# Performance work log

Measured on AMD Instinct MI355X. Metric: run time of the kernel, lower is better.

Reference implementation:

```python
import jax, jax.numpy as jnp
import numpy as np

B, N, NS, D, H, DH, K, R = 16, 4096, 24, 512, 8, 64, 512, 8
ITERS = 3
EPS = 1e-8
LORA_SCALE = 8.0


def setup_inputs() -> dict:
    key = jax.random.key(0)
    ks = jax.random.split(key, 16)
    rn = lambda k, shape, s=0.02: jax.random.normal(k, shape, jnp.float32) * s
    return {
        "inputs": jax.random.normal(ks[0], (B, N, D), jnp.float32),
        "conditioning": jax.random.normal(ks[1], (B, NS, D), jnp.float32),
        "Wq": rn(ks[2], (D, D)),
        "Wk": rn(ks[3], (D, D)),
        "Wv": rn(ks[4], (D, D)),
        "gru_w_ih": rn(ks[5], (3 * D, D)),
        "gru_w_hh": rn(ks[6], (3 * D, D)),
        "gru_b_ih": jnp.zeros((3 * D,), jnp.float32),
        "gru_b_hh": jnp.zeros((3 * D,), jnp.float32),
        "ln_in_g": jnp.ones((D,), jnp.float32),
        "ln_in_b": jnp.zeros((D,), jnp.float32),
        "ln_s_g": jnp.ones((D,), jnp.float32),
        "ln_s_b": jnp.zeros((D,), jnp.float32),
        "ln_f_g": jnp.ones((D,), jnp.float32),
        "ln_f_b": jnp.zeros((D,), jnp.float32),
        "W1": rn(ks[7], (D, 4 * D)),
        "b1": jnp.zeros((4 * D,), jnp.float32),
        "W2": rn(ks[8], (4 * D, D)),
        "b2": jnp.zeros((D,), jnp.float32),
        "A1": rn(ks[9], (K, D, R)),
        "B1": rn(ks[10], (K, R, 4 * D)),
        "A2": rn(ks[11], (K, 4 * D, R)),
        "B2": rn(ks[12], (K, R, D)),
        "codebook": jax.random.normal(ks[13], (K, D), jnp.float32),
    }


def _ln(x, g, b):
    m = x.mean(-1, keepdims=True)
    v = ((x - m) ** 2).mean(-1, keepdims=True)
    return (x - m) * jax.lax.rsqrt(v + 1e-5) * g + b


def _lora(x, idx, A, Bm):
    # AdaLoRA: per-slot adapter selected by VQ index.  idx: [b, ns] int
    t = jnp.einsum('bnd,bndr->bnr', x, A[idx])          # [b,ns,r]
    return jnp.einsum('bnr,bnro->bno', t, Bm[idx]) * (LORA_SCALE / R)


def _vq(slots, codebook):
    d2 = (jnp.sum(slots ** 2, -1, keepdims=True)
          - 2.0 * jnp.einsum('bnd,kd->bnk', slots, codebook)
          + jnp.sum(codebook ** 2, -1))                 # [b,ns,K]
    idx = jnp.argmin(d2, axis=-1)                       # [b,ns]
    q = codebook[idx]
    commit = jnp.mean((slots - jax.lax.stop_gradient(q)) ** 2)
    return idx, commit


def _gru(x, h, w_ih, w_hh, b_ih, b_hh):
    gi = x @ w_ih.T + b_ih
    gh = h @ w_hh.T + b_hh
    ir, iz, inn = jnp.split(gi, 3, axis=-1)
    hr, hz, hn = jnp.split(gh, 3, axis=-1)
    r = jax.nn.sigmoid(ir + hr)
    z = jax.nn.sigmoid(iz + hz)
    n = jnp.tanh(inn + r * hn)
    return (1.0 - z) * n + z * h


def reference(inputs, conditioning, Wq, Wk, Wv, gru_w_ih, gru_w_hh, gru_b_ih,
              gru_b_hh, ln_in_g, ln_in_b, ln_s_g, ln_s_b, ln_f_g, ln_f_b,
              W1, b1, W2, b2, A1, B1, A2, B2, codebook):
    scale = DH ** -0.5
    x = _ln(inputs, ln_in_g, ln_in_b)
    # mod_position='f': k/v/q LoRAs are ZeroModule, so k/v are identical
    # across iterations -> compute once (same math as the torch loop).
    k = (x @ Wk).reshape(B, N, H, DH)
    v = (x @ Wv).reshape(B, N, H, DH)
    slots = conditioning
    indices = None
    commit = jnp.float32(0.0)
    for i in range(ITERS):
        idx = None
        if i > 0:
            indices, commit = _vq(slots, codebook)
            idx = indices
        slots_prev = slots
        s = _ln(slots, ln_s_g, ln_s_b)
        q = (s @ Wq).reshape(B, NS, H, DH)
        dots = jnp.einsum('bihd,bjhd->bihj', q, k) * scale      # [b,ns,h,n]
        a = jax.nn.softmax(dots.reshape(B, NS * H, N), axis=1).reshape(B, NS, H, N)
        attn_bw = a
        a = a + EPS
        a = a / a.sum(-1, keepdims=True)
        upd = jnp.einsum('bjhd,bihj->bihd', v, a).reshape(B * NS, D)
        slots = _gru(upd, slots_prev.reshape(B * NS, D),
                     gru_w_ih, gru_w_hh, gru_b_ih, gru_b_hh).reshape(B, NS, D)
        slots_prev_ff = slots
        s2 = _ln(slots, ln_f_g, ln_f_b)
        h1 = s2 @ W1 + b1
        if idx is not None:
            h1 = h1 + _lora(s2, idx, A1, B1)
        h1 = jax.nn.relu(h1)
        out = h1 @ W2 + b2
        if idx is not None:
            out = out + _lora(h1, idx, A2, B2)
        slots = out + slots_prev_ff
        attn = attn_bw.mean(axis=2)                              # [b,ns,n]
    return slots, attn, indices, commit, indices
```

## Files before the change

### kernel.cpp

```cpp
#include <hip/hip_runtime.h>
#include <hip/hip_bf16.h>
#include <math.h>


#define B_ 16
#define N_ 4096
#define NS_ 24
#define D_ 512
#define H_ 8
#define DH_ 64
#define KC_ 512
#define R_ 8
#define TT_ (NS_*H_)
#define EPS_ 1e-8f
#define BNSD_ (B_*NS_*D_)
#define M_ 384

typedef unsigned short u16x8 __attribute__((ext_vector_type(8)));
typedef short s16x8 __attribute__((ext_vector_type(8)));
typedef float f32x4 __attribute__((ext_vector_type(4)));

__device__ inline unsigned short f2bf(float f) {
  unsigned int u = __float_as_uint(f);
  u += 0x7FFFu + ((u >> 16) & 1u);
  return (unsigned short)(u >> 16);
}
__device__ inline float bf2f(unsigned short h) {
  return __uint_as_float(((unsigned int)h) << 16);
}

__global__ __launch_bounds__(128) void ln_hl_kernel(const float* __restrict__ X,
    const float* __restrict__ g, const float* __restrict__ bb,
    unsigned short* __restrict__ Y)
{
  int row = blockIdx.x;
  const float* xr = X + (size_t)row * D_;
  int t = threadIdx.x;
  float lv[4];
#pragma unroll
  for (int i = 0; i < 4; ++i) lv[i] = xr[t + 128 * i];
  float s = lv[0] + lv[1] + lv[2] + lv[3];
#pragma unroll
  for (int o = 1; o < 64; o <<= 1) s += __shfl_xor(s, o);
  __shared__ float sh[2], sh2[2];
  if ((t & 63) == 0) sh[t >> 6] = s;
  __syncthreads();
  float mean = (sh[0] + sh[1]) * (1.f / D_);
  float q = 0.f;
#pragma unroll
  for (int i = 0; i < 4; ++i) { float d = lv[i] - mean; q += d * d; }
#pragma unroll
  for (int o = 1; o < 64; o <<= 1) q += __shfl_xor(q, o);
  if ((t & 63) == 0) sh2[t >> 6] = q;
  __syncthreads();
  float var = (sh2[0] + sh2[1]) * (1.f / D_);
  float rstd = 1.0f / sqrtf(var + 1e-5f);
#pragma unroll
  for (int i = 0; i < 4; ++i) {
    int d = t + 128 * i;
    float y = (lv[i] - mean) * rstd * g[d] + bb[d];
    unsigned short h = f2bf(y);
    unsigned short l = f2bf(y - bf2f(h));
    Y[(size_t)row * 1024 + d] = h;
    Y[(size_t)row * 1024 + 512 + d] = l;
  }
}

__global__ __launch_bounds__(128) void ln_dual_kernel(const float* __restrict__ X,
    const float* __restrict__ g, const float* __restrict__ bb,
    float* __restrict__ Yf, unsigned short* __restrict__ Yhl)
{
  int row = blockIdx.x;
  const float* xr = X + (size_t)row * D_;
  int t = threadIdx.x;
  float lv[4];
#pragma unroll
  for (int i = 0; i < 4; ++i) lv[i] = xr[t + 128 * i];
  float s = lv[0] + lv[1] + lv[2] + lv[3];
#pragma unroll
  for (int o = 1; o < 64; o <<= 1) s += __shfl_xor(s, o);
  __shared__ float sh[2], sh2[2];
  if ((t & 63) == 0) sh[t >> 6] = s;
  __syncthreads();
  float mean = (sh[0] + sh[1]) * (1.f / D_);
  float q = 0.f;
#pragma unroll
  for (int i = 0; i < 4; ++i) { float d = lv[i] - mean; q += d * d; }
#pragma unroll
  for (int o = 1; o < 64; o <<= 1) q += __shfl_xor(q, o);
  if ((t & 63) == 0) sh2[t >> 6] = q;
  __syncthreads();
  float var = (sh2[0] + sh2[1]) * (1.f / D_);
  float rstd = 1.0f / sqrtf(var + 1e-5f);
#pragma unroll
  for (int i = 0; i < 4; ++i) {
    int d = t + 128 * i;
    float y = (lv[i] - mean) * rstd * g[d] + bb[d];
    Yf[(size_t)row * D_ + d] = y;
    unsigned short h = f2bf(y);
    unsigned short l = f2bf(y - bf2f(h));
    Yhl[(size_t)row * 1024 + d] = h;
    Yhl[(size_t)row * 1024 + 512 + d] = l;
  }
}

__global__ __launch_bounds__(256) void wtrans_g(const float* __restrict__ W,
    unsigned short* __restrict__ WT, int K, int N)
{
  __shared__ float t[64][65];
  int n0 = blockIdx.x * 64, k0 = blockIdx.y * 64;
  for (int e = threadIdx.x; e < 4096; e += 256) {
    int kk = e >> 6, nn = e & 63;
    t[kk][nn] = W[(size_t)(k0 + kk) * N + n0 + nn];
  }
  __syncthreads();
  for (int e = threadIdx.x; e < 4096; e += 256) {
    int nn = e >> 6, kk = e & 63;
    float v = t[kk][nn];
    unsigned short h = f2bf(v);
    unsigned short l = f2bf(v - bf2f(h));
    size_t base = (size_t)(n0 + nn) * 3 * K + (k0 + kk);
    WT[base] = h; WT[base + K] = h; WT[base + 2 * K] = l;
  }
}

__global__ __launch_bounds__(256) void wsplit_nm(const float* __restrict__ W,
    unsigned short* __restrict__ WT, int K, int total)
{
  int e = blockIdx.x * 256 + threadIdx.x;
  if (e >= total) return;
  int n = e / K, k = e % K;
  float v = W[e];
  unsigned short h = f2bf(v);
  unsigned short l = f2bf(v - bf2f(h));
  size_t base = (size_t)n * 3 * K + k;
  WT[base] = h; WT[base + K] = h; WT[base + 2 * K] = l;
}

__global__ __launch_bounds__(256) void f32tohl_kernel(const float* __restrict__ X,
    float* __restrict__ Cout, unsigned short* __restrict__ HL, int total)
{
  int e = blockIdx.x * 256 + threadIdx.x;
  if (e >= total) return;
  float v = X[e];
  if (Cout) Cout[e] = v;
  int m = e >> 9, d = e & 511;
  unsigned short h = f2bf(v);
  unsigned short l = f2bf(v - bf2f(h));
  HL[(size_t)m * 1024 + d] = h;
  HL[(size_t)m * 1024 + 512 + d] = l;
}

__global__ __launch_bounds__(256) void reluhl_kernel(const float* __restrict__ X,
    unsigned short* __restrict__ HL)
{
  int e = blockIdx.x * 256 + threadIdx.x;
  float v = fmaxf(X[e], 0.f);
  int m = e >> 11, d = e & 2047;
  unsigned short h = f2bf(v);
  unsigned short l = f2bf(v - bf2f(h));
  HL[(size_t)m * 4096 + d] = h;
  HL[(size_t)m * 4096 + 2048 + d] = l;
}

__global__ __launch_bounds__(256) void gemm_kv(
    const unsigned short* __restrict__ A, const unsigned short* __restrict__ BT,
    float* __restrict__ C)
{
  __shared__ unsigned short As[128 * 64];
  __shared__ unsigned short Bs[128 * 64];
  const int tid = threadIdx.x;
  const int lane = tid & 63, wid = tid >> 6;
  const int wm = wid >> 1, wn = wid & 1;
  const int g = lane >> 4, r16 = lane & 15;
  const int m0 = blockIdx.y * 128, n0 = blockIdx.x * 128;

  f32x4 acc[4][4] = {};
  u16x8 ra[4], rb[4];
  int srow[4], sj[4];
#pragma unroll
  for (int i = 0; i < 4; ++i) {
    int s = tid + (i << 8);
    srow[i] = s >> 3;
    sj[i] = (s & 7) ^ (srow[i] & 7);
  }
#pragma unroll
  for (int i = 0; i < 4; ++i) {
    ra[i] = *(const u16x8*)(A + (size_t)(m0 + srow[i]) * 1024 + (sj[i] << 3));
    rb[i] = *(const u16x8*)(BT + (size_t)(n0 + srow[i]) * 1536 + (sj[i] << 3));
  }
  u16x8* Asw = (u16x8*)As;
  u16x8* Bsw = (u16x8*)Bs;
  const s16x8* Asv = (const s16x8*)As;
  const s16x8* Bsv = (const s16x8*)Bs;

  for (int kk = 0; kk < 24; ++kk) {
    __syncthreads();
#pragma unroll
    for (int i = 0; i < 4; ++i) {
      Asw[tid + (i << 8)] = ra[i];
      Bsw[tid + (i << 8)] = rb[i];
    }
    __syncthreads();
    if (kk + 1 < 24) {
      int k2 = kk + 1;
      int acol = ((k2 < 16) ? k2 : (k2 - 16)) * 64;
      int bcol = k2 * 64;
#pragma unroll
      for (int i = 0; i < 4; ++i) {
        ra[i] = *(const u16x8*)(A + (size_t)(m0 + srow[i]) * 1024 + acol + (sj[i] << 3));
        rb[i] = *(const u16x8*)(BT + (size_t)(n0 + srow[i]) * 1536 + bcol + (sj[i] << 3));
      }
    }
#pragma unroll
    for (int kh = 0; kh < 2; ++kh) {
      s16x8 af[4], bfr[4];
      int j = kh * 4 + g;
#pragma unroll
      for (int mi = 0; mi < 4; ++mi) {
        int m = wm * 64 + mi * 16 + r16;
        af[mi] = Asv[m * 8 + (j ^ (m & 7))];
      }
#pragma unroll
      for (int ni = 0; ni < 4; ++ni) {
        int n = wn * 64 + ni * 16 + r16;
        bfr[ni] = Bsv[n * 8 + (j ^ (n & 7))];
      }
#pragma unroll
      for (int mi = 0; mi < 4; ++mi)
#pragma unroll
        for (int ni = 0; ni < 4; ++ni)
          acc[mi][ni] = __builtin_amdgcn_mfma_f32_16x16x32_bf16(
              af[mi], bfr[ni], acc[mi][ni], 0, 0, 0);
    }
  }
#pragma unroll
  for (int mi = 0; mi < 4; ++mi) {
    int mrow = m0 + wm * 64 + mi * 16 + g * 4;
#pragma unroll
    for (int ni = 0; ni < 4; ++ni) {
      int ncol = n0 + wn * 64 + ni * 16 + r16;
#pragma unroll
      for (int j = 0; j < 4; ++j)
        C[(size_t)(mrow + j) * 512 + ncol] = acc[mi][ni][j];
    }
  }
}

__global__ __launch_bounds__(256) void gemm_sp(
    const unsigned short* __restrict__ A, const unsigned short* __restrict__ WT,
    float* __restrict__ part, int N, int K, int S)
{
  __shared__ unsigned short As[128 * 64];
  __shared__ unsigned short Bs[64 * 64];
  const int tid = threadIdx.x;
  const int lane = tid & 63, wid = tid >> 6;
  const int wm = wid >> 1, wn = wid & 1;
  const int g = lane >> 4, r16 = lane & 15;
  const int n0 = blockIdx.x * 64, m0 = blockIdx.y * 128, z = blockIdx.z;
  const int twoK = 2 * K;
  const size_t ldb = (size_t)3 * K;

  f32x4 acc[4][2] = {};
  u16x8 ra[4], rb[2];
  int arow[4], aj[4], brow[2], bj[2];
#pragma unroll
  for (int i = 0; i < 4; ++i) {
    int s = tid + (i << 8);
    arow[i] = s >> 3; aj[i] = (s & 7) ^ (arow[i] & 7);
  }
#pragma unroll
  for (int i = 0; i < 2; ++i) {
    int s = tid + (i << 8);
    brow[i] = s >> 3; bj[i] = (s & 7) ^ (brow[i] & 7);
  }
  const int s0 = z * S;
  {
    int c = s0 * 64;
    int ac = (c < twoK) ? c : c - twoK;
#pragma unroll
    for (int i = 0; i < 4; ++i)
      ra[i] = *(const u16x8*)(A + (size_t)(m0 + arow[i]) * twoK + ac + (aj[i] << 3));
#pragma unroll
    for (int i = 0; i < 2; ++i)
      rb[i] = *(const u16x8*)(WT + (size_t)(n0 + brow[i]) * ldb + c + (bj[i] << 3));
  }
  u16x8* Asw = (u16x8*)As;
  u16x8* Bsw = (u16x8*)Bs;
  const s16x8* Asv = (const s16x8*)As;
  const s16x8* Bsv = (const s16x8*)Bs;

  for (int st = 0; st < S; ++st) {
    __syncthreads();
#pragma unroll
    for (int i = 0; i < 4; ++i) Asw[tid + (i << 8)] = ra[i];
#pragma unroll
    for (int i = 0; i < 2; ++i) Bsw[tid + (i << 8)] = rb[i];
    __syncthreads();
    if (st + 1 < S) {
      int c = (s0 + st + 1) * 64;
      int ac = (c < twoK) ? c : c - twoK;
#pragma unroll
      for (int i = 0; i < 4; ++i)
        ra[i] = *(const u16x8*)(A + (size_t)(m0 + arow[i]) * twoK + ac + (aj[i] << 3));
#pragma unroll
      for (int i = 0; i < 2; ++i)
        rb[i] = *(const u16x8*)(WT + (size_t)(n0 + brow[i]) * ldb + c + (bj[i] << 3));
    }
#pragma unroll
    for (int kh = 0; kh < 2; ++kh) {
      int j = kh * 4 + g;
      s16x8 af[4], bf2v[2];
#pragma unroll
      for (int mi = 0; mi < 4; ++mi) {
        int m = wm * 64 + mi * 16 + r16;
        af[mi] = Asv[m * 8 + (j ^ (m & 7))];
      }
#pragma unroll
      for (int ni = 0; ni < 2; ++ni) {
        int n = wn * 32 + ni * 16 + r16;
        bf2v[ni] = Bsv[n * 8 + (j ^ (n & 7))];
      }
#pragma unroll
      for (int mi = 0; mi < 4; ++mi)
#pragma unroll
        for (int ni = 0; ni < 2; ++ni)
          acc[mi][ni] = __builtin_amdgcn_mfma_f32_16x16x32_bf16(
              af[mi], bf2v[ni], acc[mi][ni], 0, 0, 0);
    }
  }
  size_t zb = (size_t)z * M_ * N;
#pragma unroll
  for (int mi = 0; mi < 4; ++mi) {
    int mr = m0 + wm * 64 + mi * 16 + g * 4;
#pragma unroll
    for (int ni = 0; ni < 2; ++ni) {
      int nc = n0 + wn * 32 + ni * 16 + r16;
#pragma unroll
      for (int j2 = 0; j2 < 4; ++j2)
        part[zb + (size_t)(mr + j2) * N + nc] = acc[mi][ni][j2];
    }
  }
}

template<bool BIAS, bool RES, bool WHL>
__global__ __launch_bounds__(256) void redep(const float* __restrict__ part,
    const float* __restrict__ bias, const float* __restrict__ res,
    float* __restrict__ C, unsigned short* __restrict__ HL, int N, int Z)
{
  int e = blockIdx.x * 256 + threadIdx.x;
  size_t MN = (size_t)M_ * N;
  float v = 0.f;
  for (int z = 0; z < Z; ++z) v += part[(size_t)z * MN + e];
  int m = e / N, n = e - m * N;
  if (BIAS) v += bias[n];
  if (RES) v += res[e];
  C[e] = v;
  if (WHL) {
    unsigned short h = f2bf(v), l = f2bf(v - bf2f(h));
    HL[(size_t)m * 2 * N + n] = h;
    HL[(size_t)m * 2 * N + N + n] = l;
  }
}

__global__ __launch_bounds__(256) void vsum_kernel(const float* __restrict__ v,
                                                   float* __restrict__ vsum)
{
  int b = blockIdx.x >> 3, h = blockIdx.x & 7;
  int dh = threadIdx.x & 63, w = threadIdx.x >> 6;
  float acc = 0.f;
  for (int j = w * (N_ / 4); j < (w + 1) * (N_ / 4); ++j)
    acc += v[((size_t)b * N_ + j) * D_ + h * 64 + dh];
  __shared__ float sh[4][64];
  sh[w][dh] = acc;
  __syncthreads();
  if (w == 0)
    vsum[(size_t)blockIdx.x * 64 + dh] = sh[0][dh] + sh[1][dh] + sh[2][dh] + sh[3][dh];
}

__global__ __launch_bounds__(256) void vq_kernel(const float* __restrict__ slots,
    const float* __restrict__ cb, int* __restrict__ idx, float* __restrict__ commit)
{
  __shared__ float ss[D_];
  int slot = blockIdx.x;
  const float* sr = slots + (size_t)slot * D_;
  for (int d = threadIdx.x; d < D_; d += 256) ss[d] = sr[d];
  __syncthreads();
  float best = 1e30f; int bi = 0;
  for (int c = threadIdx.x; c < KC_; c += 256) {
    const float* cr = cb + (size_t)c * D_;
    float d2 = 0.f;
    for (int d = 0; d < D_; ++d) { float df = ss[d] - cr[d]; d2 += df * df; }
    if (d2 < best) { best = d2; bi = c; }
  }
  __shared__ float rb[256]; __shared__ int ri[256];
  rb[threadIdx.x] = best; ri[threadIdx.x] = bi;
  __syncthreads();
  for (int s = 128; s > 0; s >>= 1) {
    if (threadIdx.x < s) {
      float ob = rb[threadIdx.x + s]; int oi = ri[threadIdx.x + s];
      if (ob < rb[threadIdx.x] || (ob == rb[threadIdx.x] && oi < ri[threadIdx.x])) {
        rb[threadIdx.x] = ob; ri[threadIdx.x] = oi;
      }
    }
    __syncthreads();
  }
  if (threadIdx.x == 0) {
    idx[slot] = ri[0];
    atomicAdd(commit, rb[0] * (1.f / (B_ * NS_ * D_)));
  }
}

__global__ __launch_bounds__(256) void dots_kernel(const float* __restrict__ q,
    const float* __restrict__ k, float* __restrict__ dots)
{
  int b = blockIdx.y >> 3, h = blockIdx.y & 7;
  int j0 = blockIdx.x * 64;
  __shared__ float qs[NS_][DH_];
  __shared__ float ks[64][DH_ + 1];
  for (int e = threadIdx.x; e < NS_ * DH_; e += 256) {
    int i = e >> 6, dh = e & 63;
    qs[i][dh] = q[(size_t)(b * NS_ + i) * D_ + h * 64 + dh];
  }
  for (int e = threadIdx.x; e < 64 * 64; e += 256) {
    int jj = e >> 6, dh = e & 63;
    ks[jj][dh] = k[((size_t)b * N_ + j0 + jj) * D_ + h * 64 + dh];
  }
  __syncthreads();
  int jj = threadIdx.x & 63;
  int ib = threadIdx.x >> 6;
  float acc[6] = {0.f, 0.f, 0.f, 0.f, 0.f, 0.f};
  for (int dh = 0; dh < 64; ++dh) {
    float kv = ks[jj][dh];
#pragma unroll
    for (int ii = 0; ii < 6; ++ii) acc[ii] += qs[ii * 4 + ib][dh] * kv;
  }
#pragma unroll
  for (int ii = 0; ii < 6; ++ii) {
    int i = ii * 4 + ib;
    dots[((size_t)(b * NS_ + i) * H_ + h) * N_ + j0 + jj] = acc[ii] * 0.125f;
  }
}

__global__ __launch_bounds__(256) void softmax_kernel(float* __restrict__ dots,
    float* __restrict__ asum, float* __restrict__ attn)
{
  int b = blockIdx.y;
  int j = blockIdx.x * 256 + threadIdx.x;
  size_t base = (size_t)b * TT_ * N_ + j;
  float m = -1e30f;
  for (int t = 0; t < TT_; ++t) m = fmaxf(m, dots[base + (size_t)t * N_]);
  float S = 0.f;
  for (int t = 0; t < TT_; ++t) S += __expf(dots[base + (size_t)t * N_] - m);
  float rinv = 1.f / S;
  float am[NS_];
#pragma unroll
  for (int i = 0; i < NS_; ++i) am[i] = 0.f;
  for (int t = 0; t < TT_; ++t) {
    float w = __expf(dots[base + (size_t)t * N_] - m) * rinv;
    dots[base + (size_t)t * N_] = w;
    am[t >> 3] += w;
    float wsum = w;
#pragma unroll
    for (int o = 1; o < 64; o <<= 1) wsum += __shfl_xor(wsum, o);
    if ((threadIdx.x & 63) == 0) atomicAdd(&asum[b * TT_ + t], wsum);
  }
  if (attn) {
    for (int i = 0; i < NS_; ++i)
      attn[((size_t)b * NS_ + i) * N_ + j] = am[i] * (1.f / H_);
  }
}

__global__ __launch_bounds__(256) void upd_part_kernel(const float* __restrict__ a,
    const float* __restrict__ v, float* __restrict__ part)
{
  int bh = blockIdx.x;
  int c = blockIdx.y;
  int b = bh >> 3, h = bh & 7;
  __shared__ float vs[64][DH_ + 1];
  __shared__ float as[NS_][64];
  int dh = threadIdx.x & 63;
  int ib = threadIdx.x >> 6;
  float acc[6] = {0.f, 0.f, 0.f, 0.f, 0.f, 0.f};
  for (int j0 = c * 1024; j0 < (c + 1) * 1024; j0 += 64) {
    __syncthreads();
    for (int e = threadIdx.x; e < 64 * 64; e += 256) {
      int jj = e >> 6, d2 = e & 63;
      vs[jj][d2] = v[((size_t)b * N_ + j0 + jj) * D_ + h * 64 + d2];
    }
    for (int e = threadIdx.x; e < NS_ * 64; e += 256) {
      int i = e >> 6, jj = e & 63;
      as[i][jj] = a[((size_t)(b * NS_ + i) * H_ + h) * N_ + j0 + jj];
    }
    __syncthreads();
    for (int jj = 0; jj < 64; ++jj) {
      float vv = vs[jj][dh];
#pragma unroll
      for (int ii = 0; ii < 6; ++ii) acc[ii] += as[ii * 4 + ib][jj] * vv;
    }
  }
#pragma unroll
  for (int ii = 0; ii < 6; ++ii) {
    int i = ii * 4 + ib;
    part[((size_t)c * B_ * NS_ + b * NS_ + i) * D_ + h * 64 + dh] = acc[ii];
  }
}

__global__ __launch_bounds__(256) void upd_fin_kernel(const float* __restrict__ part,
    const float* __restrict__ vsum, const float* __restrict__ asum,
    unsigned short* __restrict__ updhl)
{
  int e = blockIdx.x * 256 + threadIdx.x;
  int d = e & 511, bi = e >> 9;
  int b = bi / NS_, h = d >> 6, dh = d & 63;
  float s = part[e] + part[BNSD_ + e] + part[2 * BNSD_ + e] + part[3 * BNSD_ + e];
  float dnm = asum[bi * H_ + h] + (float)N_ * EPS_;
  float val = (s + EPS_ * vsum[(b * H_ + h) * 64 + dh]) / dnm;
  unsigned short hh = f2bf(val), ll = f2bf(val - bf2f(hh));
  updhl[(size_t)bi * 1024 + d] = hh;
  updhl[(size_t)bi * 1024 + 512 + d] = ll;
}

__global__ __launch_bounds__(256) void gru_kernel(const float* __restrict__ gi,
    const float* __restrict__ gh, const float* __restrict__ h, float* __restrict__ out)
{
  int e = blockIdx.x * 256 + threadIdx.x;
  int row = e >> 9, d = e & 511;
  const float* gir = gi + (size_t)row * 1536;
  const float* ghr = gh + (size_t)row * 1536;
  float ir = gir[d], iz = gir[512 + d], inn = gir[1024 + d];
  float hr = ghr[d], hz = ghr[512 + d], hn = ghr[1024 + d];
  float r = 1.f / (1.f + __expf(-(ir + hr)));
  float z = 1.f / (1.f + __expf(-(iz + hz)));
  float n = tanhf(inn + r * hn);
  out[e] = (1.f - z) * n + z * h[e];
}

template<bool RELU_X>
__global__ __launch_bounds__(256) void lora_kernel(const float* __restrict__ x,
    const float* __restrict__ Am, const float* __restrict__ Bm,
    const int* __restrict__ idx, float* __restrict__ out, int Din, int Dout)
{
  int slot = blockIdx.x;
  int code = idx[slot];
  const float* xr = x + (size_t)slot * Din;
  const float* Ar = Am + (size_t)code * Din * R_;
  const float* Br = Bm + (size_t)code * R_ * Dout;
  float part[R_];
#pragma unroll
  for (int r = 0; r < R_; ++r) part[r] = 0.f;
  for (int d = threadIdx.x; d < Din; d += 256) {
    float xv = xr[d];
    if (RELU_X) xv = fmaxf(xv, 0.f);
#pragma unroll
    for (int r = 0; r < R_; ++r) part[r] += xv * Ar[(size_t)d * R_ + r];
  }
#pragma unroll
  for (int r = 0; r < R_; ++r)
#pragma unroll
    for (int o = 1; o < 64; o <<= 1) part[r] += __shfl_xor(part[r], o);
  __shared__ float tsh[4][R_];
  __shared__ float tfin[R_];
  int wave = threadIdx.x >> 6, lane = threadIdx.x & 63;
  if (lane == 0)
    for (int r = 0; r < R_; ++r) tsh[wave][r] = part[r];
  __syncthreads();
  if (threadIdx.x < R_)
    tfin[threadIdx.x] = (tsh[0][threadIdx.x] + tsh[1][threadIdx.x] +
                         tsh[2][threadIdx.x] + tsh[3][threadIdx.x]);
  __syncthreads();
  for (int c = threadIdx.x; c < Dout; c += 256) {
    float acc = 0.f;
#pragma unroll
    for (int r = 0; r < R_; ++r) acc += tfin[r] * Br[(size_t)r * Dout + c];
    out[(size_t)slot * Dout + c] += acc;
  }
}

__global__ __launch_bounds__(256) void finalize_kernel(const float* __restrict__ slots,
    const int* __restrict__ idx, const float* __restrict__ commit, float* __restrict__ out)
{
  int t = blockIdx.x * 256 + threadIdx.x;
  if (t < B_ * NS_ * D_) out[t] = slots[t];
  if (t < B_ * NS_) {
    float iv = (float)idx[t];
    out[1769472 + t] = iv;
    out[1769857 + t] = iv;
  }
  if (t == 0) out[1769856] = commit[0];
}

extern "C" void kernel_launch(void* const* d_in, const int* in_sizes, int n_in,
                              void* d_out, int out_size, void* d_ws, size_t ws_size,
                              hipStream_t stream)
{
  const float* inputs  = (const float*)d_in[0];
  const float* cond    = (const float*)d_in[1];
  const float* Wq      = (const float*)d_in[2];
  const float* Wk      = (const float*)d_in[3];
  const float* Wv      = (const float*)d_in[4];
  const float* w_ih    = (const float*)d_in[5];
  const float* w_hh    = (const float*)d_in[6];
  const float* b_ih    = (const float*)d_in[7];
  const float* b_hh    = (const float*)d_in[8];
  const float* ln_in_g = (const float*)d_in[9];
  const float* ln_in_b = (const float*)d_in[10];
  const float* ln_s_g  = (const float*)d_in[11];
  const float* ln_s_b  = (const float*)d_in[12];
  const float* ln_f_g  = (const float*)d_in[13];
  const float* ln_f_b  = (const float*)d_in[14];
  const float* W1      = (const float*)d_in[15];
  const float* b1      = (const float*)d_in[16];
  const float* W2      = (const float*)d_in[17];
  const float* b2      = (const float*)d_in[18];
  const float* A1      = (const float*)d_in[19];
  const float* B1m     = (const float*)d_in[20];
  const float* A2      = (const float*)d_in[21];
  const float* B2m     = (const float*)d_in[22];
  const float* codebook= (const float*)d_in[23];

  float* out = (float*)d_out;
  float* ws  = (float*)d_ws;

  unsigned short* xhat_hl = (unsigned short*)ws;
  float* dots    = ws;
  float* updpart = ws + 12582912;
  float* gpart   = ws + 13369344;
  unsigned short* WqT  = (unsigned short*)(ws + 16515072);
  unsigned short* wihT = (unsigned short*)(ws + 16908288);
  unsigned short* whhT = (unsigned short*)(ws + 18087936);
  unsigned short* W1T  = (unsigned short*)(ws + 19267584);
  unsigned short* W2T  = (unsigned short*)(ws + 20840448);
  unsigned short* s_hl    = (unsigned short*)(ws + 22413312);
  unsigned short* slotshl = (unsigned short*)(ws + 22609920);
  unsigned short* updhl   = (unsigned short*)(ws + 22806528);
  unsigned short* h1hl    = (unsigned short*)(ws + 23003136);

  size_t off = 33554432;
  float* kbuf = ws + off; off += 33554432;
  float* vbuf = ws + off; off += 33554432;
  unsigned short* WkT = (unsigned short*)(ws + off); off += 393216;
  unsigned short* WvT = (unsigned short*)(ws + off); off += 393216;
  float* slots_cur = ws + off; off += BNSD_;
  float* slots_gru = ws + off; off += BNSD_;
  float* sbuf      = ws + off; off += BNSD_;
  float* qb        = ws + off; off += BNSD_;
  float* gib       = ws + off; off += B_ * NS_ * 3 * D_;
  float* ghb       = ws + off; off += B_ * NS_ * 3 * D_;
  float* h1b       = ws + off; off += B_ * NS_ * 4 * D_;
  float* vsumb     = ws + off; off += B_ * H_ * DH_;
  float* asumb     = ws + off; off += B_ * TT_;
  float* commitb   = ws + off; off += 1;
  int*   idxb      = (int*)(ws + off); off += B_ * NS_;

  ln_hl_kernel<<<B_ * N_, 128, 0, stream>>>(inputs, ln_in_g, ln_in_b, xhat_hl);
  wtrans_g<<<dim3(8, 8), 256, 0, stream>>>(Wk, WkT, 512, 512);
  wtrans_g<<<dim3(8, 8), 256, 0, stream>>>(Wv, WvT, 512, 512);
  gemm_kv<<<dim3(4, 512), 256, 0, stream>>>(xhat_hl, WkT, kbuf);
  gemm_kv<<<dim3(4, 512), 256, 0, stream>>>(xhat_hl, WvT, vbuf);
  vsum_kernel<<<B_ * H_, 256, 0, stream>>>(vbuf, vsumb);
  wtrans_g<<<dim3(8, 8), 256, 0, stream>>>(Wq, WqT, 512, 512);
  wsplit_nm<<<3072, 256, 0, stream>>>(w_ih, wihT, 512, 1536 * 512);
  wsplit_nm<<<3072, 256, 0, stream>>>(w_hh, whhT, 512, 1536 * 512);
  wtrans_g<<<dim3(32, 8), 256, 0, stream>>>(W1, W1T, 512, 2048);
  wtrans_g<<<dim3(8, 32), 256, 0, stream>>>(W2, W2T, 2048, 512);
  f32tohl_kernel<<<768, 256, 0, stream>>>(cond, slots_cur, slotshl, BNSD_);

  for (int it = 0; it < 3; ++it) {
    if (it > 0) {
      hipMemsetAsync(commitb, 0, sizeof(float), stream);
      vq_kernel<<<B_ * NS_, 256, 0, stream>>>(slots_cur, codebook, idxb, commitb);
    }
    ln_dual_kernel<<<B_ * NS_, 128, 0, stream>>>(slots_cur, ln_s_g, ln_s_b, sbuf, s_hl);
    gemm_sp<<<dim3(8, 3, 4), 256, 0, stream>>>(s_hl, WqT, gpart, 512, 512, 6);
    redep<false, false, false><<<768, 256, 0, stream>>>(gpart, nullptr, nullptr, qb, nullptr, 512, 4);
    dots_kernel<<<dim3(N_ / 64, B_ * H_), 256, 0, stream>>>(qb, kbuf, dots);
    hipMemsetAsync(asumb, 0, (size_t)B_ * TT_ * sizeof(float), stream);
    softmax_kernel<<<dim3(N_ / 256, B_), 256, 0, stream>>>(
        dots, asumb, (it == 2) ? (out + (size_t)BNSD_) : nullptr);
    upd_part_kernel<<<dim3(B_ * H_, 4), 256, 0, stream>>>(dots, vbuf, updpart);
    upd_fin_kernel<<<BNSD_ / 256, 256, 0, stream>>>(updpart, vsumb, asumb, updhl);
    gemm_sp<<<dim3(24, 3, 4), 256, 0, stream>>>(updhl, wihT, gpart, 1536, 512, 6);
    redep<true, false, false><<<2304, 256, 0, stream>>>(gpart, b_ih, nullptr, gib, nullptr, 1536, 4);
    gemm_sp<<<dim3(24, 3, 4), 256, 0, stream>>>(slotshl, whhT, gpart, 1536, 512, 6);
    redep<true, false, false><<<2304, 256, 0, stream>>>(gpart, b_hh, nullptr, ghb, nullptr, 1536, 4);
    gru_kernel<<<BNSD_ / 256, 256, 0, stream>>>(gib, ghb, slots_cur, slots_gru);
    ln_dual_kernel<<<B_ * NS_, 128, 0, stream>>>(slots_gru, ln_f_g, ln_f_b, sbuf, s_hl);
    gemm_sp<<<dim3(32, 3, 4), 256, 0, stream>>>(s_hl, W1T, gpart, 2048, 512, 6);
    redep<true, false, false><<<3072, 256, 0, stream>>>(gpart, b1, nullptr, h1b, nullptr, 2048, 4);
    if (it > 0)
      lora_kernel<false><<<B_ * NS_, 256, 0, stream>>>(sbuf, A1, B1m, idxb, h1b, D_, 4 * D_);
    reluhl_kernel<<<3072, 256, 0, stream>>>(h1b, h1hl);
    gemm_sp<<<dim3(8, 3, 8), 256, 0, stream>>>(h1hl, W2T, gpart, 512, 2048, 12);
    redep<true, true, true><<<768, 256, 0, stream>>>(gpart, b2, slots_gru, slots_cur, slotshl, 512, 8);
    if (it > 0)
      lora_kernel<true><<<B_ * NS_, 256, 0, stream>>>(h1b, A2, B2m, idxb, slots_cur, 4 * D_, D_);
    if (it == 1)
      f32tohl_kernel<<<768, 256, 0, stream>>>(slots_cur, nullptr, slotshl, BNSD_);
  }

  finalize_kernel<<<BNSD_ / 256, 256, 0, stream>>>(slots_cur, idxb, commitb, out);
}
```

Baseline: 2.003 ms.

## Split softmax over slot groups, move row sums to separate kernel, widen upd split

```diff
diff --git a/kernel.cpp b/kernel.cpp
--- a/kernel.cpp
+++ b/kernel.cpp
@@ -443,32 +443,62 @@
 }
 
 __global__ __launch_bounds__(256) void softmax_kernel(float* __restrict__ dots,
-    float* __restrict__ asum, float* __restrict__ attn)
+    float* __restrict__ attn)
 {
   int b = blockIdx.y;
-  int j = blockIdx.x * 256 + threadIdx.x;
+  int jj = threadIdx.x & 63;
+  int tg = threadIdx.x >> 6;
+  int j = blockIdx.x * 64 + jj;
   size_t base = (size_t)b * TT_ * N_ + j;
+  const int t0 = tg * 48;
+  __shared__ float red[4][64];
+
   float m = -1e30f;
-  for (int t = 0; t < TT_; ++t) m = fmaxf(m, dots[base + (size_t)t * N_]);
+  for (int t = t0; t < t0 + 48; ++t)
+    m = fmaxf(m, dots[base + (size_t)t * N_]);
+  red[tg][jj] = m;
+  __syncthreads();
+  m = fmaxf(fmaxf(red[0][jj], red[1][jj]), fmaxf(red[2][jj], red[3][jj]));
+  __syncthreads();
+
   float S = 0.f;
-  for (int t = 0; t < TT_; ++t) S += __expf(dots[base + (size_t)t * N_] - m);
+  for (int t = t0; t < t0 + 48; ++t)
+    S += __expf(dots[base + (size_t)t * N_] - m);
+  red[tg][jj] = S;
+  __syncthreads();
+  S = red[0][jj] + red[1][jj] + red[2][jj] + red[3][jj];
   float rinv = 1.f / S;
-  float am[NS_];
-#pragma unroll
-  for (int i = 0; i < NS_; ++i) am[i] = 0.f;
-  for (int t = 0; t < TT_; ++t) {
-    float w = __expf(dots[base + (size_t)t * N_] - m) * rinv;
-    dots[base + (size_t)t * N_] = w;
-    am[t >> 3] += w;
-    float wsum = w;
-#pragma unroll
-    for (int o = 1; o < 64; o <<= 1) wsum += __shfl_xor(wsum, o);
-    if ((threadIdx.x & 63) == 0) atomicAdd(&asum[b * TT_ + t], wsum);
-  }
-  if (attn) {
-    for (int i = 0; i < NS_; ++i)
-      attn[((size_t)b * NS_ + i) * N_ + j] = am[i] * (1.f / H_);
-  }
+
+  for (int s6 = 0; s6 < 6; ++s6) {
+    float am = 0.f;
+#pragma unroll
+    for (int r = 0; r < 8; ++r) {
+      int t = t0 + s6 * 8 + r;
+      float w = __expf(dots[base + (size_t)t * N_] - m) * rinv;
+      dots[base + (size_t)t * N_] = w;
+      am += w;
+    }
+    if (attn)
+      attn[((size_t)b * NS_ + (tg * 6 + s6)) * N_ + j] = am * (1.f / H_);
+  }
+}
+
+__global__ __launch_bounds__(256) void asum_kernel(const float* __restrict__ w,
+                                                   float* __restrict__ asum)
+{
+  int row = blockIdx.x;
+  const float4* r4 = (const float4*)(w + (size_t)row * N_);
+  float s = 0.f;
+  for (int p = threadIdx.x; p < N_ / 4; p += 256) {
+    float4 v = r4[p];
+    s += v.x + v.y + v.z + v.w;
+  }
+#pragma unroll
+  for (int o = 1; o < 64; o <<= 1) s += __shfl_xor(s, o);
+  __shared__ float sh[4];
+  if ((threadIdx.x & 63) == 0) sh[threadIdx.x >> 6] = s;
+  __syncthreads();
+  if (threadIdx.x == 0) asum[row] = sh[0] + sh[1] + sh[2] + sh[3];
 }
 
 __global__ __launch_bounds__(256) void upd_part_kernel(const float* __restrict__ a,
@@ -482,7 +512,7 @@
   int dh = threadIdx.x & 63;
   int ib = threadIdx.x >> 6;
   float acc[6] = {0.f, 0.f, 0.f, 0.f, 0.f, 0.f};
-  for (int j0 = c * 1024; j0 < (c + 1) * 1024; j0 += 64) {
+  for (int j0 = c * 512; j0 < (c + 1) * 512; j0 += 64) {
     __syncthreads();
     for (int e = threadIdx.x; e < 64 * 64; e += 256) {
       int jj = e >> 6, d2 = e & 63;
@@ -513,7 +543,9 @@
   int e = blockIdx.x * 256 + threadIdx.x;
   int d = e & 511, bi = e >> 9;
   int b = bi / NS_, h = d >> 6, dh = d & 63;
-  float s = part[e] + part[BNSD_ + e] + part[2 * BNSD_ + e] + part[3 * BNSD_ + e];
+  float s = 0.f;
+#pragma unroll
+  for (int z = 0; z < 8; ++z) s += part[(size_t)z * BNSD_ + e];
   float dnm = asum[bi * H_ + h] + (float)N_ * EPS_;
   float val = (s + EPS_ * vsum[(b * H_ + h) * 64 + dh]) / dnm;
   unsigned short hh = f2bf(val), ll = f2bf(val - bf2f(hh));
@@ -625,16 +657,16 @@
   unsigned short* xhat_hl = (unsigned short*)ws;
   float* dots    = ws;
   float* updpart = ws + 12582912;
-  float* gpart   = ws + 13369344;
-  unsigned short* WqT  = (unsigned short*)(ws + 16515072);
-  unsigned short* wihT = (unsigned short*)(ws + 16908288);
-  unsigned short* whhT = (unsigned short*)(ws + 18087936);
-  unsigned short* W1T  = (unsigned short*)(ws + 19267584);
-  unsigned short* W2T  = (unsigned short*)(ws + 20840448);
-  unsigned short* s_hl    = (unsigned short*)(ws + 22413312);
-  unsigned short* slotshl = (unsigned short*)(ws + 22609920);
-  unsigned short* updhl   = (unsigned short*)(ws + 22806528);
-  unsigned short* h1hl    = (unsigned short*)(ws + 23003136);
+  float* gpart   = ws + 14155776;
+  unsigned short* WqT  = (unsigned short*)(ws + 17301504);
+  unsigned short* wihT = (unsigned short*)(ws + 17694720);
+  unsigned short* whhT = (unsigned short*)(ws + 18874368);
+  unsigned short* W1T  = (unsigned short*)(ws + 20054016);
+  unsigned short* W2T  = (unsigned short*)(ws + 21626880);
+  unsigned short* s_hl    = (unsigned short*)(ws + 23199744);
+  unsigned short* slotshl = (unsigned short*)(ws + 23396352);
+  unsigned short* updhl   = (unsigned short*)(ws + 23592960);
+  unsigned short* h1hl    = (unsigned short*)(ws + 23789568);
 
   size_t off = 33554432;
   float* kbuf = ws + off; off += 33554432;
@@ -675,10 +707,10 @@
     gemm_sp<<<dim3(8, 3, 4), 256, 0, stream>>>(s_hl, WqT, gpart, 512, 512, 6);
     redep<false, false, false><<<768, 256, 0, stream>>>(gpart, nullptr, nullptr, qb, nullptr, 512, 4);
     dots_kernel<<<dim3(N_ / 64, B_ * H_), 256, 0, stream>>>(qb, kbuf, dots);
-    hipMemsetAsync(asumb, 0, (size_t)B_ * TT_ * sizeof(float), stream);
-    softmax_kernel<<<dim3(N_ / 256, B_), 256, 0, stream>>>(
-        dots, asumb, (it == 2) ? (out + (size_t)BNSD_) : nullptr);
-    upd_part_kernel<<<dim3(B_ * H_, 4), 256, 0, stream>>>(dots, vbuf, updpart);
+    softmax_kernel<<<dim3(N_ / 64, B_), 256, 0, stream>>>(
+        dots, (it == 2) ? (out + (size_t)BNSD_) : nullptr);
+    asum_kernel<<<B_ * TT_, 256, 0, stream>>>(dots, asumb);
+    upd_part_kernel<<<dim3(B_ * H_, 8), 256, 0, stream>>>(dots, vbuf, updpart);
     upd_fin_kernel<<<BNSD_ / 256, 256, 0, stream>>>(updpart, vsumb, asumb, updhl);
     gemm_sp<<<dim3(24, 3, 4), 256, 0, stream>>>(updhl, wihT, gpart, 1536, 512, 6);
     redep<true, false, false><<<2304, 256, 0, stream>>>(gpart, b_ih, nullptr, gib, nullptr, 1536, 4);
```

After: 1.654 ms. -17.4%, faster.
